# Kernel tuning notes

Measured on AMD Instinct MI355X. Metric: run time of the kernel, lower is better.

The kernel has to match this reference:

```python
import jax, jax.numpy as jnp
import numpy as np
from jax import lax

B, C, O, K, L, W = 32, 128, 128, 3, 4096, 1
PAD, DIL = 1, 1


def _conv(x, w, b):
    # x: [B,C,H,W], w: [O,C,K,1] -> [B,O,H,W] (zeros padding, stride 1)
    y = lax.conv_general_dilated(x, w, window_strides=(1, 1),
                                 padding=[(PAD, PAD), (0, 0)],
                                 rhs_dilation=(DIL, 1),
                                 dimension_numbers=('NCHW', 'OIHW', 'NCHW'))
    return y + b[None, :, None, None]


def setup_inputs() -> dict:
    key = jax.random.key(0)
    ks = jax.random.split(key, 6)
    x = jax.random.normal(ks[0], (B, C, L, W), dtype=jnp.float32)
    # offset/modulator convs are zero-init in torch; use small random values to
    # exercise the deformable gather path (represents a trained state)
    w_off = jax.random.normal(ks[1], (2 * K, C, K, 1), dtype=jnp.float32) * 0.01
    b_off = jax.random.normal(ks[2], (2 * K,), dtype=jnp.float32) * 0.1
    w_mod = jax.random.normal(ks[3], (K, C, K, 1), dtype=jnp.float32) * 0.01
    b_mod = jax.random.normal(ks[4], (K,), dtype=jnp.float32) * 0.1
    w_reg = jax.random.normal(ks[5], (O, C, K, 1), dtype=jnp.float32) * (1.0 / np.sqrt(C * K))
    return {"x": x, "w_off": w_off, "b_off": b_off,
            "w_mod": w_mod, "b_mod": b_mod, "w_reg": w_reg}


def reference(x, w_off, b_off, w_mod, b_mod, w_reg):
    b, c, h, w = x.shape
    max_offset = max(h, w) / 4.0
    offset = jnp.clip(_conv(x, w_off, b_off), -max_offset, max_offset)  # [B,2K,H,W]
    mask = 2.0 * jax.nn.sigmoid(_conv(x, w_mod, b_mod))                 # [B,K,H,W]

    off = offset.reshape(b, K, 2, h, w)
    off_y, off_x = off[:, :, 0], off[:, :, 1]                           # [B,K,H,W]

    # sampling positions (stride=1, pad_w=0, kw=1)
    base_y = (-PAD + jnp.arange(K, dtype=jnp.float32)[:, None] * DIL
              + jnp.arange(h, dtype=jnp.float32)[None, :])              # [K,H]
    py = base_y[None, :, :, None] + off_y                               # [B,K,H,W]
    px = jnp.arange(w, dtype=jnp.float32)[None, None, None, :] + off_x  # [B,K,H,W]

    y0 = jnp.floor(py); x0 = jnp.floor(px)
    iy0 = y0.astype(jnp.int32); ix0 = x0.astype(jnp.int32)
    wy1 = py - y0; wy0 = 1.0 - wy1
    wx1 = px - x0; wx0 = 1.0 - wx1

    def gather(iy, ix):
        iyc = jnp.clip(iy, 0, h - 1)
        ixc = jnp.clip(ix, 0, w - 1)
        # per-batch gather: xb [C,H,W], idx [K,H,W] -> [C,K,H,W]
        return jax.vmap(lambda xb, yb, xb_i: xb[:, yb, xb_i])(x, iyc, ixc)

    acc = jnp.zeros((b, c, K, h, w), dtype=x.dtype)
    corners = [(iy0, ix0, wy0 * wx0), (iy0, ix0 + 1, wy0 * wx1),
               (iy0 + 1, ix0, wy1 * wx0), (iy0 + 1, ix0 + 1, wy1 * wx1)]
    for iy, ix, wgt in corners:
        valid = ((iy >= 0) & (iy < h) & (ix >= 0) & (ix < w)).astype(x.dtype)
        acc = acc + gather(iy, ix) * (wgt * valid)[:, None]  # [B,C,K,H,W]

    val = acc * mask[:, None]                                 # modulated samples
    out = jnp.einsum('bckhw,ock->bohw', val, w_reg[:, :, :, 0])
    return out
```

## Files before the change

kernel.cpp:

```cpp
#include <hip/hip_runtime.h>
#include <hip/hip_bf16.h>
#include <math.h>


typedef __attribute__((ext_vector_type(8))) short bf16x8;
typedef __attribute__((ext_vector_type(4))) float f32x4;
typedef float f32x2u __attribute__((ext_vector_type(2), aligned(4)));

#define WIN 160
#define WPAD 161

static __device__ inline unsigned short f2bf(float f) {
    __hip_bfloat16 h = __float2bfloat16(f);
    union { __hip_bfloat16 b; unsigned short u; } cv;
    cv.b = h;
    return cv.u;
}

__global__ __launch_bounds__(256) void k_wra(const float* __restrict__ w_reg,
                                             const float* __restrict__ w_off,
                                             const float* __restrict__ w_mod,
                                             unsigned short* __restrict__ WrA,
                                             float* __restrict__ wT) {
    int t = blockIdx.x * 256 + threadIdx.x;
    if (t < 8 * 12 * 64 * 8) {
        int e  = t & 7;
        int l  = (t >> 3) & 63;
        int ms = t >> 9;
        int m  = ms / 12;
        int s  = ms - m * 12;
        int o  = m * 16 + (l & 15);
        int kc = s * 32 + ((l >> 4) & 3) * 8 + e;
        int tap = kc >> 7;
        int c   = kc & 127;
        WrA[t] = f2bf(w_reg[(o * 128 + c) * 3 + tap]);
    } else if (t < 8 * 12 * 64 * 8 + 128 * 27) {
        int u = t - 8 * 12 * 64 * 8;
        int c = u / 27, r = u - c * 27;
        int ch = r / 3, tap = r - ch * 3;
        wT[c * 32 + r] = (ch < 6) ? w_off[(ch * 128 + c) * 3 + tap]
                                  : w_mod[((ch - 6) * 128 + c) * 3 + tap];
    }
}

__global__ __launch_bounds__(512) void k_prep(const float* __restrict__ x,
                                              const float* __restrict__ wT,
                                              const float* __restrict__ b_off,
                                              const float* __restrict__ b_mod,
                                              int* __restrict__ addr2,
                                              float* __restrict__ wae,
                                              float* __restrict__ wbe) {
    __shared__ float red[7 * 64 * 19];
    int t = threadIdx.x;
    int lane = t & 63;
    int wv = t >> 6;
    int b = blockIdx.y;
    int i = blockIdx.x * 128 + lane * 2;

    int c0 = __builtin_amdgcn_readfirstlane(wv) * 16;

    float acc[18];
#pragma unroll
    for (int z = 0; z < 18; ++z) acc[z] = 0.f;

    const float* xr = x + (size_t)b * 524288 + (size_t)c0 * 4096;
    const float* wbase = wT + c0 * 32;
#pragma unroll 2
    for (int c = 0; c < 16; ++c) {
        const float* row = xr + (size_t)c * 4096;
        f32x2u v = *(const f32x2u*)(row + i);
        float lm = row[max(i - 1, 0)];
        float rp = row[min(i + 2, 4095)];
        float left  = (i > 0)        ? lm : 0.f;
        float right = (i + 2 < 4096) ? rp : 0.f;
        const float* wrow = wbase + c * 32;
#pragma unroll
        for (int ch = 0; ch < 9; ++ch) {
            float w0 = wrow[ch * 3 + 0];
            float w1 = wrow[ch * 3 + 1];
            float w2 = wrow[ch * 3 + 2];
            acc[ch * 2 + 0] += left * w0 + v.x * w1 + v.y  * w2;
            acc[ch * 2 + 1] += v.x  * w0 + v.y * w1 + right * w2;
        }
    }

    if (wv > 0) {
        float* r = &red[((wv - 1) * 64 + lane) * 19];
#pragma unroll
        for (int z = 0; z < 18; ++z) r[z] = acc[z];
    }
    __syncthreads();
    if (wv != 0) return;

#pragma unroll
    for (int p = 0; p < 7; ++p) {
        const float* r = &red[(p * 64 + lane) * 19];
#pragma unroll
        for (int z = 0; z < 18; ++z) acc[z] += r[z];
    }

#pragma unroll
    for (int k = 0; k < 3; ++k) {
        int   av[2];
        float wav[2], wbv[2];
#pragma unroll
        for (int ii = 0; ii < 2; ++ii) {
            float offy = acc[(2 * k) * 2 + ii]     + b_off[2 * k];
            float offx = acc[(2 * k + 1) * 2 + ii] + b_off[2 * k + 1];
            offy = fminf(fmaxf(offy, -1024.f), 1024.f);
            offx = fminf(fmaxf(offx, -1024.f), 1024.f);
            float am = acc[(6 + k) * 2 + ii] + b_mod[k];
            float m  = 2.f / (1.f + expf(-am));

            float py = (float)(i + ii - 1 + k) + offy;
            float y0 = floorf(py);
            int   iy0 = (int)y0;
            float wy1 = py - y0, wy0 = 1.f - wy1;
            float x0f = floorf(offx);
            int   ix0 = (int)x0f;
            float wx1 = offx - x0f, wx0 = 1.f - wx1;

            float sx = (ix0 == 0) ? wx0 : ((ix0 == -1) ? wx1 : 0.f);
            float scal = m * sx;

            float wAv = (iy0 >= 0 && iy0 < 4096)  ? scal * wy0 : 0.f;
            float wBv = (iy0 >= -1 && iy0 < 4095) ? scal * wy1 : 0.f;

            int addr = min(max(iy0, 0), 4094);
            bool eq = (iy0 == addr);
            wav[ii] = eq ? wAv : (iy0 == -1   ? wBv : 0.f);
            wbv[ii] = eq ? wBv : (iy0 == 4095 ? wAv : 0.f);
            av[ii] = addr;
        }
        int j = (b * 3 + k) * 4096 + i;
        *(int2*)(addr2 + j)  = make_int2(av[0], av[1]);
        *(f32x2u*)(wae + j)  = (f32x2u){wav[0], wav[1]};
        *(f32x2u*)(wbe + j)  = (f32x2u){wbv[0], wbv[1]};
    }
}

__global__ __launch_bounds__(512) void k_fused(const unsigned short* __restrict__ WrA,
                                               const float* __restrict__ x,
                                               const int* __restrict__ addr2,
                                               const float* __restrict__ wae,
                                               const float* __restrict__ wbe,
                                               float* __restrict__ out) {
    __shared__ float win[32 * WPAD];
    int t = threadIdx.x;
    int l = t & 63;
    int w = t >> 6;
    int b  = blockIdx.y;
    int ib = blockIdx.x;
    int q = l >> 4;
    int il = l & 15;
    int f0 = ib * 8 + w;
    int i0 = f0 * 16 + il;
    int i0t = ib * 128;
    int wsod = i0t - 16;
    if (wsod > 4096 - WIN) wsod = 4096 - WIN;
    if (wsod < 0) wsod = 0;
    const float* xb = x + (size_t)b * 524288;
    const bf16x8* Ag = (const bf16x8*)WrA;

    int   a_[3];
    float wa_[3], wb_[3];
    bool  okw[3];
#pragma unroll
    for (int k = 0; k < 3; ++k) {
        int j = (b * 3 + k) * 4096 + i0;
        int a = addr2[j];
        a_[k]  = a;
        wa_[k] = wae[j];
        wb_[k] = wbe[j];
        okw[k] = (bool)__all(a >= wsod && a <= wsod + WIN - 2);
    }

    f32x4 acc[8];
#pragma unroll
    for (int m = 0; m < 8; ++m) acc[m] = (f32x4){0.f, 0.f, 0.f, 0.f};

    for (int cc = 0; cc < 4; ++cc) {
        int cb = cc * 32;
        __syncthreads();
#pragma unroll
        for (int it = 0; it < 3; ++it) {
            int idx = it * 512 + t;
            if (idx < 1280) {
                int r  = idx / 40;
                int cp = idx - r * 40;
                float4 v = *(const float4*)(xb + (size_t)(cb + r) * 4096 + wsod + cp * 4);
                float* dst = &win[r * WPAD + cp * 4];
                dst[0] = v.x; dst[1] = v.y; dst[2] = v.z; dst[3] = v.w;
            }
        }
        __syncthreads();

#pragma unroll
        for (int k = 0; k < 3; ++k) {
            int s = k * 4 + cc;
            float v[8];
            float wa = wa_[k], wb = wb_[k];
            if (okw[k]) {
                int pos = a_[k] - wsod;
#pragma unroll
                for (int e = 0; e < 8; ++e) {
                    const float* base = &win[(q * 8 + e) * WPAD + pos];
                    v[e] = wa * base[0] + wb * base[1];
                }
            } else {
                int a = a_[k];
#pragma unroll
                for (int e = 0; e < 8; ++e) {
                    const float* row = xb + (size_t)(cb + q * 8 + e) * 4096;
                    f32x2u p2 = *(const f32x2u*)(row + a);
                    v[e] = wa * p2.x + wb * p2.y;
                }
            }
            bf16x8 Bv;
#pragma unroll
            for (int e = 0; e < 8; ++e) Bv[e] = (short)f2bf(v[e]);
#pragma unroll
            for (int m = 0; m < 8; ++m) {
                bf16x8 A = Ag[(m * 12 + s) * 64 + l];
                acc[m] = __builtin_amdgcn_mfma_f32_16x16x32_bf16(A, Bv, acc[m], 0, 0, 0);
            }
        }
    }

    int r0 = q * 4;
#pragma unroll
    for (int m = 0; m < 8; ++m) {
#pragma unroll
        for (int r = 0; r < 4; ++r) {
            int o = m * 16 + r0 + r;
            out[((size_t)(b * 128 + o)) * 4096 + i0] = acc[m][r];
        }
    }
}

extern "C" void kernel_launch(void* const* d_in, const int* in_sizes, int n_in,
                              void* d_out, int out_size, void* d_ws, size_t ws_size,
                              hipStream_t stream) {
    const float* x     = (const float*)d_in[0];
    const float* w_off = (const float*)d_in[1];
    const float* b_off = (const float*)d_in[2];
    const float* w_mod = (const float*)d_in[3];
    const float* b_mod = (const float*)d_in[4];
    const float* w_reg = (const float*)d_in[5];
    float* out = (float*)d_out;

    char* ws = (char*)d_ws;
    unsigned short* WrA = (unsigned short*)(ws);
    float* wT    = (float*)(ws + 98304);
    int*   addr2 = (int*)  (ws + 131072);
    float* wae   = (float*)(ws + 1703936);
    float* wbe   = (float*)(ws + 3276800);

    k_wra<<<206, 256, 0, stream>>>(w_reg, w_off, w_mod, WrA, wT);
    k_prep<<<dim3(32, 32), 512, 0, stream>>>(x, wT, b_off, b_mod,
                                             addr2, wae, wbe);
    k_fused<<<dim3(32, 32), 512, 0, stream>>>(WrA, x, addr2, wae, wbe, out);
}
```

Before: 77.97 us.

## Share sampled B tiles via LDS and assign output-channel tiles per wave

Each wave now writes its interpolated bf16 B fragments into a double-buffered LDS array. Every wave then holds only its own 16-output-channel slice of the weights in registers and runs MFMAs over all 8 position tiles. Weight traffic per wave drops from all 8 A tiles to 3 register-resident fragments per channel chunk. The next x window is also prefetched into registers while the MFMAs run, so the global load overlaps compute. The cost is extra LDS space, LDS round-trips for B, and an extra barrier per chunk.

```diff
diff --git a/kernel.cpp b/kernel.cpp
--- a/kernel.cpp
+++ b/kernel.cpp
@@ -146,6 +146,7 @@
                                                const float* __restrict__ wbe,
                                                float* __restrict__ out) {
     __shared__ float win[32 * WPAD];
+    __shared__ short Bl[2][8][3][512];
     int t = threadIdx.x;
     int l = t & 63;
     int w = t >> 6;
@@ -153,9 +154,8 @@
     int ib = blockIdx.x;
     int q = l >> 4;
     int il = l & 15;
-    int f0 = ib * 8 + w;
-    int i0 = f0 * 16 + il;
     int i0t = ib * 128;
+    int i0p = i0t + w * 16 + il;
     int wsod = i0t - 16;
     if (wsod > 4096 - WIN) wsod = 4096 - WIN;
     if (wsod < 0) wsod = 0;
@@ -167,7 +167,7 @@
     bool  okw[3];
 #pragma unroll
     for (int k = 0; k < 3; ++k) {
-        int j = (b * 3 + k) * 4096 + i0;
+        int j = (b * 3 + k) * 4096 + i0p;
         int a = addr2[j];
         a_[k]  = a;
         wa_[k] = wae[j];
@@ -177,27 +177,32 @@
 
     f32x4 acc[8];
 #pragma unroll
-    for (int m = 0; m < 8; ++m) acc[m] = (f32x4){0.f, 0.f, 0.f, 0.f};
+    for (int f = 0; f < 8; ++f) acc[f] = (f32x4){0.f, 0.f, 0.f, 0.f};
+
+#pragma unroll
+    for (int it = 0; it < 3; ++it) {
+        int idx = it * 512 + t;
+        if (idx < 1280) {
+            int r  = idx / 40;
+            int cp = idx - r * 40;
+            float4 v = *(const float4*)(xb + (size_t)r * 4096 + wsod + cp * 4);
+            float* dst = &win[r * WPAD + cp * 4];
+            dst[0] = v.x; dst[1] = v.y; dst[2] = v.z; dst[3] = v.w;
+        }
+    }
+    __syncthreads();
 
     for (int cc = 0; cc < 4; ++cc) {
+        int p  = cc & 1;
         int cb = cc * 32;
-        __syncthreads();
-#pragma unroll
-        for (int it = 0; it < 3; ++it) {
-            int idx = it * 512 + t;
-            if (idx < 1280) {
-                int r  = idx / 40;
-                int cp = idx - r * 40;
-                float4 v = *(const float4*)(xb + (size_t)(cb + r) * 4096 + wsod + cp * 4);
-                float* dst = &win[r * WPAD + cp * 4];
-                dst[0] = v.x; dst[1] = v.y; dst[2] = v.z; dst[3] = v.w;
-            }
-        }
-        __syncthreads();
+
+        bf16x8 Areg[3];
+#pragma unroll
+        for (int k = 0; k < 3; ++k)
+            Areg[k] = Ag[(w * 12 + k * 4 + cc) * 64 + l];
 
 #pragma unroll
         for (int k = 0; k < 3; ++k) {
-            int s = k * 4 + cc;
             float v[8];
             float wa = wa_[k], wb = wb_[k];
             if (okw[k]) {
@@ -219,21 +224,56 @@
             bf16x8 Bv;
 #pragma unroll
             for (int e = 0; e < 8; ++e) Bv[e] = (short)f2bf(v[e]);
-#pragma unroll
-            for (int m = 0; m < 8; ++m) {
-                bf16x8 A = Ag[(m * 12 + s) * 64 + l];
-                acc[m] = __builtin_amdgcn_mfma_f32_16x16x32_bf16(A, Bv, acc[m], 0, 0, 0);
+            *(bf16x8*)&Bl[p][w][k][l * 8] = Bv;
+        }
+
+        float4 stg[3];
+        if (cc < 3) {
+            const float* src = xb + (size_t)(cb + 32) * 4096;
+#pragma unroll
+            for (int it = 0; it < 3; ++it) {
+                int idx = it * 512 + t;
+                if (idx < 1280) {
+                    int r  = idx / 40;
+                    int cp = idx - r * 40;
+                    stg[it] = *(const float4*)(src + (size_t)r * 4096 + wsod + cp * 4);
+                }
             }
         }
+        __syncthreads();
+
+#pragma unroll
+        for (int f = 0; f < 8; ++f) {
+#pragma unroll
+            for (int k = 0; k < 3; ++k) {
+                bf16x8 Bv = *(const bf16x8*)&Bl[p][f][k][l * 8];
+                acc[f] = __builtin_amdgcn_mfma_f32_16x16x32_bf16(Areg[k], Bv, acc[f], 0, 0, 0);
+            }
+        }
+
+        if (cc < 3) {
+#pragma unroll
+            for (int it = 0; it < 3; ++it) {
+                int idx = it * 512 + t;
+                if (idx < 1280) {
+                    int r  = idx / 40;
+                    int cp = idx - r * 40;
+                    float* dst = &win[r * WPAD + cp * 4];
+                    dst[0] = stg[it].x; dst[1] = stg[it].y;
+                    dst[2] = stg[it].z; dst[3] = stg[it].w;
+                }
+            }
+            __syncthreads();
+        }
     }
 
     int r0 = q * 4;
 #pragma unroll
-    for (int m = 0; m < 8; ++m) {
+    for (int f = 0; f < 8; ++f) {
 #pragma unroll
         for (int r = 0; r < 4; ++r) {
-            int o = m * 16 + r0 + r;
-            out[((size_t)(b * 128 + o)) * 4096 + i0] = acc[m][r];
+            int o = w * 16 + r0 + r;
+            out[((size_t)(b * 128 + o)) * 4096 + i0t + f * 16 + il] = acc[f][r];
         }
     }
 }
```

Result: faster. 66.65 us (-14.5%).

## Fuse offset/mask conv into main kernel via MFMA and restructure GEMM over output channels

Applied to the files above, without the earlier changes.

Removes the separate prep kernel and computes the offset/modulator 3-tap conv inside the main kernel using bf16 MFMA on an LDS window of all 128 channels. This drops the addr/weight round trip through global memory and a launch. The main GEMM now has each wave own 16 output channels, with the sampled B tiles shared through double-buffered LDS, so A fragments are loaded once per wave. The trade-offs are much higher LDS usage (about 100KB), which lowers occupancy, and bf16 rounding in the offset conv, which can shift the floor of sampling positions.

```diff
diff --git a/kernel.cpp b/kernel.cpp
--- a/kernel.cpp
+++ b/kernel.cpp
@@ -21,9 +21,9 @@
                                              const float* __restrict__ w_off,
                                              const float* __restrict__ w_mod,
                                              unsigned short* __restrict__ WrA,
-                                             float* __restrict__ wT) {
+                                             unsigned short* __restrict__ WcA) {
     int t = blockIdx.x * 256 + threadIdx.x;
-    if (t < 8 * 12 * 64 * 8) {
+    if (t < 49152) {
         int e  = t & 7;
         int l  = (t >> 3) & 63;
         int ms = t >> 9;
@@ -34,178 +34,160 @@
         int tap = kc >> 7;
         int c   = kc & 127;
         WrA[t] = f2bf(w_reg[(o * 128 + c) * 3 + tap]);
-    } else if (t < 8 * 12 * 64 * 8 + 128 * 27) {
-        int u = t - 8 * 12 * 64 * 8;
-        int c = u / 27, r = u - c * 27;
-        int ch = r / 3, tap = r - ch * 3;
-        wT[c * 32 + r] = (ch < 6) ? w_off[(ch * 128 + c) * 3 + tap]
-                                  : w_mod[((ch - 6) * 128 + c) * 3 + tap];
-    }
-}
-
-__global__ __launch_bounds__(512) void k_prep(const float* __restrict__ x,
-                                              const float* __restrict__ wT,
-                                              const float* __restrict__ b_off,
-                                              const float* __restrict__ b_mod,
-                                              int* __restrict__ addr2,
-                                              float* __restrict__ wae,
-                                              float* __restrict__ wbe) {
-    __shared__ float red[7 * 64 * 19];
-    int t = threadIdx.x;
-    int lane = t & 63;
-    int wv = t >> 6;
-    int b = blockIdx.y;
-    int i = blockIdx.x * 128 + lane * 2;
-
-    int c0 = __builtin_amdgcn_readfirstlane(wv) * 16;
-
-    float acc[18];
-#pragma unroll
-    for (int z = 0; z < 18; ++z) acc[z] = 0.f;
-
-    const float* xr = x + (size_t)b * 524288 + (size_t)c0 * 4096;
-    const float* wbase = wT + c0 * 32;
-#pragma unroll 2
-    for (int c = 0; c < 16; ++c) {
-        const float* row = xr + (size_t)c * 4096;
-        f32x2u v = *(const f32x2u*)(row + i);
-        float lm = row[max(i - 1, 0)];
-        float rp = row[min(i + 2, 4095)];
-        float left  = (i > 0)        ? lm : 0.f;
-        float right = (i + 2 < 4096) ? rp : 0.f;
-        const float* wrow = wbase + c * 32;
-#pragma unroll
-        for (int ch = 0; ch < 9; ++ch) {
-            float w0 = wrow[ch * 3 + 0];
-            float w1 = wrow[ch * 3 + 1];
-            float w2 = wrow[ch * 3 + 2];
-            acc[ch * 2 + 0] += left * w0 + v.x * w1 + v.y  * w2;
-            acc[ch * 2 + 1] += v.x  * w0 + v.y * w1 + right * w2;
-        }
-    }
-
-    if (wv > 0) {
-        float* r = &red[((wv - 1) * 64 + lane) * 19];
-#pragma unroll
-        for (int z = 0; z < 18; ++z) r[z] = acc[z];
-    }
-    __syncthreads();
-    if (wv != 0) return;
-
-#pragma unroll
-    for (int p = 0; p < 7; ++p) {
-        const float* r = &red[(p * 64 + lane) * 19];
-#pragma unroll
-        for (int z = 0; z < 18; ++z) acc[z] += r[z];
-    }
-
-#pragma unroll
-    for (int k = 0; k < 3; ++k) {
-        int   av[2];
-        float wav[2], wbv[2];
-#pragma unroll
-        for (int ii = 0; ii < 2; ++ii) {
-            float offy = acc[(2 * k) * 2 + ii]     + b_off[2 * k];
-            float offx = acc[(2 * k + 1) * 2 + ii] + b_off[2 * k + 1];
-            offy = fminf(fmaxf(offy, -1024.f), 1024.f);
-            offx = fminf(fmaxf(offx, -1024.f), 1024.f);
-            float am = acc[(6 + k) * 2 + ii] + b_mod[k];
-            float m  = 2.f / (1.f + expf(-am));
-
-            float py = (float)(i + ii - 1 + k) + offy;
-            float y0 = floorf(py);
-            int   iy0 = (int)y0;
-            float wy1 = py - y0, wy0 = 1.f - wy1;
-            float x0f = floorf(offx);
-            int   ix0 = (int)x0f;
-            float wx1 = offx - x0f, wx0 = 1.f - wx1;
-
-            float sx = (ix0 == 0) ? wx0 : ((ix0 == -1) ? wx1 : 0.f);
-            float scal = m * sx;
-
-            float wAv = (iy0 >= 0 && iy0 < 4096)  ? scal * wy0 : 0.f;
-            float wBv = (iy0 >= -1 && iy0 < 4095) ? scal * wy1 : 0.f;
-
-            int addr = min(max(iy0, 0), 4094);
-            bool eq = (iy0 == addr);
-            wav[ii] = eq ? wAv : (iy0 == -1   ? wBv : 0.f);
-            wbv[ii] = eq ? wBv : (iy0 == 4095 ? wAv : 0.f);
-            av[ii] = addr;
-        }
-        int j = (b * 3 + k) * 4096 + i;
-        *(int2*)(addr2 + j)  = make_int2(av[0], av[1]);
-        *(f32x2u*)(wae + j)  = (f32x2u){wav[0], wav[1]};
-        *(f32x2u*)(wbe + j)  = (f32x2u){wbv[0], wbv[1]};
-    }
-}
-
-__global__ __launch_bounds__(512) void k_fused(const unsigned short* __restrict__ WrA,
-                                               const float* __restrict__ x,
-                                               const int* __restrict__ addr2,
-                                               const float* __restrict__ wae,
-                                               const float* __restrict__ wbe,
-                                               float* __restrict__ out) {
-    __shared__ float win[32 * WPAD];
+    } else if (t < 49152 + 6144) {
+        int u = t - 49152;
+        int e = u & 7;
+        int l = (u >> 3) & 63;
+        int s = u >> 9;
+        int o = l & 15;
+        int c   = (s & 3) * 32 + ((l >> 4) & 3) * 8 + e;
+        int tap = s >> 2;
+        float v = 0.f;
+        if (o < 6)      v = w_off[(o * 128 + c) * 3 + tap];
+        else if (o < 9) v = w_mod[((o - 6) * 128 + c) * 3 + tap];
+        WcA[u] = f2bf(v);
+    }
+}
+
+__global__ __launch_bounds__(512) void k_all(const unsigned short* __restrict__ WrA,
+                                             const unsigned short* __restrict__ WcA,
+                                             const float* __restrict__ x,
+                                             const float* __restrict__ b_off,
+                                             const float* __restrict__ b_mod,
+                                             float* __restrict__ out) {
+    __shared__ float win[4][32 * WPAD];
+    __shared__ short Bl[2][8][3][512];
+    float* convx = (float*)&Bl[0][0][0][0];
+
     int t = threadIdx.x;
     int l = t & 63;
     int w = t >> 6;
     int b  = blockIdx.y;
     int ib = blockIdx.x;
-    int q = l >> 4;
+    int q  = l >> 4;
     int il = l & 15;
-    int f0 = ib * 8 + w;
-    int i0 = f0 * 16 + il;
     int i0t = ib * 128;
     int wsod = i0t - 16;
     if (wsod > 4096 - WIN) wsod = 4096 - WIN;
     if (wsod < 0) wsod = 0;
     const float* xb = x + (size_t)b * 524288;
     const bf16x8* Ag = (const bf16x8*)WrA;
+    const bf16x8* Ac = (const bf16x8*)WcA;
+
+    int  rr_[3], co_[3];
+    bool v_[3];
+#pragma unroll
+    for (int it = 0; it < 3; ++it) {
+        int idx = it * 512 + t;
+        int r = idx / 40;
+        rr_[it] = r;
+        co_[it] = (idx - r * 40) * 4;
+        v_[it]  = (idx < 1280);
+    }
+    float4 sA[3], sB[3];
+#define LOADW(dst, cc) \
+    _Pragma("unroll") for (int it = 0; it < 3; ++it) if (v_[it]) \
+        dst[it] = *(const float4*)(xb + (size_t)((cc) * 32 + rr_[it]) * 4096 + wsod + co_[it]);
+#define WRITEW(src, cc) \
+    _Pragma("unroll") for (int it = 0; it < 3; ++it) if (v_[it]) { \
+        float* d = &win[cc][rr_[it] * WPAD + co_[it]]; \
+        d[0] = src[it].x; d[1] = src[it].y; d[2] = src[it].z; d[3] = src[it].w; }
+
+    LOADW(sA, 0) LOADW(sB, 1) WRITEW(sA, 0) LOADW(sA, 2)
+    WRITEW(sB, 1) LOADW(sB, 3) WRITEW(sA, 2) WRITEW(sB, 3)
+#undef LOADW
+#undef WRITEW
+    __syncthreads();
+
+    int gi = i0t + w * 16 + il;
+    f32x4 cv = (f32x4){0.f, 0.f, 0.f, 0.f};
+#pragma unroll
+    for (int s = 0; s < 12; ++s) {
+        int tap = s >> 2;
+        int wcc = s & 3;
+        int gk  = gi + tap - 1;
+        bool ok = (gk >= 0) && (gk < 4096);
+        int pos = gk - wsod;
+        float vv[8];
+#pragma unroll
+        for (int e = 0; e < 8; ++e)
+            vv[e] = ok ? win[wcc][(q * 8 + e) * WPAD + pos] : 0.f;
+        bf16x8 Bv;
+#pragma unroll
+        for (int e = 0; e < 8; ++e) Bv[e] = (short)f2bf(vv[e]);
+        cv = __builtin_amdgcn_mfma_f32_16x16x32_bf16(Ac[s * 64 + l], Bv, cv, 0, 0, 0);
+    }
+
+    int ilocal = w * 16 + il;
+#pragma unroll
+    for (int rr = 0; rr < 4; ++rr) {
+        int ch = q * 4 + rr;
+        if (ch < 9) convx[ch * 132 + ilocal] = cv[rr];
+    }
+    __syncthreads();
+
+    float c9[9];
+#pragma unroll
+    for (int z = 0; z < 9; ++z) c9[z] = convx[z * 132 + ilocal];
+    __syncthreads();
 
     int   a_[3];
     float wa_[3], wb_[3];
     bool  okw[3];
 #pragma unroll
     for (int k = 0; k < 3; ++k) {
-        int j = (b * 3 + k) * 4096 + i0;
-        int a = addr2[j];
-        a_[k]  = a;
-        wa_[k] = wae[j];
-        wb_[k] = wbe[j];
-        okw[k] = (bool)__all(a >= wsod && a <= wsod + WIN - 2);
+        float offy = c9[2 * k]     + b_off[2 * k];
+        float offx = c9[2 * k + 1] + b_off[2 * k + 1];
+        offy = fminf(fmaxf(offy, -1024.f), 1024.f);
+        offx = fminf(fmaxf(offx, -1024.f), 1024.f);
+        float am = c9[6 + k] + b_mod[k];
+        float m  = 2.f / (1.f + expf(-am));
+
+        float py = (float)(gi - 1 + k) + offy;
+        float y0 = floorf(py);
+        int   iy0 = (int)y0;
+        float wy1 = py - y0, wy0 = 1.f - wy1;
+        float x0f = floorf(offx);
+        int   ix0 = (int)x0f;
+        float wx1 = offx - x0f, wx0 = 1.f - wx1;
+
+        float sx = (ix0 == 0) ? wx0 : ((ix0 == -1) ? wx1 : 0.f);
+        float scal = m * sx;
+
+        float wAv = (iy0 >= 0 && iy0 < 4096)  ? scal * wy0 : 0.f;
+        float wBv = (iy0 >= -1 && iy0 < 4095) ? scal * wy1 : 0.f;
+
+        int addr = min(max(iy0, 0), 4094);
+        bool eq = (iy0 == addr);
+        wa_[k] = eq ? wAv : (iy0 == -1   ? wBv : 0.f);
+        wb_[k] = eq ? wBv : (iy0 == 4095 ? wAv : 0.f);
+        a_[k]  = addr;
+        okw[k] = (bool)__all((int)(addr >= wsod && addr <= wsod + WIN - 2));
     }
 
     f32x4 acc[8];
 #pragma unroll
-    for (int m = 0; m < 8; ++m) acc[m] = (f32x4){0.f, 0.f, 0.f, 0.f};
-
+    for (int f = 0; f < 8; ++f) acc[f] = (f32x4){0.f, 0.f, 0.f, 0.f};
+
+#pragma unroll
     for (int cc = 0; cc < 4; ++cc) {
+        int p  = cc & 1;
         int cb = cc * 32;
-        __syncthreads();
-#pragma unroll
-        for (int it = 0; it < 3; ++it) {
-            int idx = it * 512 + t;
-            if (idx < 1280) {
-                int r  = idx / 40;
-                int cp = idx - r * 40;
-                float4 v = *(const float4*)(xb + (size_t)(cb + r) * 4096 + wsod + cp * 4);
-                float* dst = &win[r * WPAD + cp * 4];
-                dst[0] = v.x; dst[1] = v.y; dst[2] = v.z; dst[3] = v.w;
-            }
-        }
-        __syncthreads();
+        bf16x8 Areg[3];
+#pragma unroll
+        for (int k = 0; k < 3; ++k)
+            Areg[k] = Ag[(w * 12 + k * 4 + cc) * 64 + l];
 
 #pragma unroll
         for (int k = 0; k < 3; ++k) {
-            int s = k * 4 + cc;
-            float v[8];
+            float vv[8];
             float wa = wa_[k], wb = wb_[k];
             if (okw[k]) {
                 int pos = a_[k] - wsod;
 #pragma unroll
                 for (int e = 0; e < 8; ++e) {
-                    const float* base = &win[(q * 8 + e) * WPAD + pos];
-                    v[e] = wa * base[0] + wb * base[1];
+                    const float* base = &win[cc][(q * 8 + e) * WPAD + pos];
+                    vv[e] = wa * base[0] + wb * base[1];
                 }
             } else {
                 int a = a_[k];
@@ -213,27 +195,35 @@
                 for (int e = 0; e < 8; ++e) {
                     const float* row = xb + (size_t)(cb + q * 8 + e) * 4096;
                     f32x2u p2 = *(const f32x2u*)(row + a);
-                    v[e] = wa * p2.x + wb * p2.y;
+                    vv[e] = wa * p2.x + wb * p2.y;
                 }
             }
             bf16x8 Bv;
 #pragma unroll
-            for (int e = 0; e < 8; ++e) Bv[e] = (short)f2bf(v[e]);
-#pragma unroll
-            for (int m = 0; m < 8; ++m) {
-                bf16x8 A = Ag[(m * 12 + s) * 64 + l];
-                acc[m] = __builtin_amdgcn_mfma_f32_16x16x32_bf16(A, Bv, acc[m], 0, 0, 0);
+            for (int e = 0; e < 8; ++e) Bv[e] = (short)f2bf(vv[e]);
+            *(bf16x8*)&Bl[p][w][k][l * 8] = Bv;
+        }
+        __syncthreads();
+
+        __builtin_amdgcn_s_setprio(1);
+#pragma unroll
+        for (int f = 0; f < 8; ++f) {
+#pragma unroll
+            for (int k = 0; k < 3; ++k) {
+                bf16x8 Bv = *(const bf16x8*)&Bl[p][f][k][l * 8];
+                acc[f] = __builtin_amdgcn_mfma_f32_16x16x32_bf16(Areg[k], Bv, acc[f], 0, 0, 0);
             }
         }
+        __builtin_amdgcn_s_setprio(0);
     }
 
     int r0 = q * 4;
 #pragma unroll
-    for (int m = 0; m < 8; ++m) {
+    for (int f = 0; f < 8; ++f) {
 #pragma unroll
         for (int r = 0; r < 4; ++r) {
-            int o = m * 16 + r0 + r;
-            out[((size_t)(b * 128 + o)) * 4096 + i0] = acc[m][r];
+            int o = w * 16 + r0 + r;
+            out[((size_t)(b * 128 + o)) * 4096 + i0t + f * 16 + il] = acc[f][r];
         }
     }
 }
@@ -251,13 +241,8 @@
 
     char* ws = (char*)d_ws;
     unsigned short* WrA = (unsigned short*)(ws);
-    float* wT    = (float*)(ws + 98304);
-    int*   addr2 = (int*)  (ws + 131072);
-    float* wae   = (float*)(ws + 1703936);
-    float* wbe   = (float*)(ws + 3276800);
-
-    k_wra<<<206, 256, 0, stream>>>(w_reg, w_off, w_mod, WrA, wT);
-    k_prep<<<dim3(32, 32), 512, 0, stream>>>(x, wT, b_off, b_mod,
-                                             addr2, wae, wbe);
-    k_fused<<<dim3(32, 32), 512, 0, stream>>>(WrA, x, addr2, wae, wbe, out);
-}
+    unsigned short* WcA = (unsigned short*)(ws + 98304);
+
+    k_wra<<<216, 256, 0, stream>>>(w_reg, w_off, w_mod, WrA, WcA);
+    k_all<<<dim3(32, 32), 512, 0, stream>>>(WrA, WcA, x, b_off, b_mod, out);
+}
```

Result: slower. 93.36 us (+19.7%).
